# Kernel tuning notes

Measured on AMD Instinct MI355X. Metric: run time of the kernel, lower is better.

## Reference

```python
import jax, jax.numpy as jnp
import numpy as np

# Problem sizes
N, D, B = 4096, 2048, 64  # nodes, feature dim, sequential samples
# LARFDSSOM hyperparameters (from __init__ defaults)
A_T = 0.3          # activation threshold
DSBETA = 1e-4      # moving-average rate
E_B = 0.5          # winner learning rate
E_N = 0.01 * E_B   # neighbor learning rate (e_n is multiplied by e_b in __init__)
EPS_DS = 0.01      # relevance smoothing


def setup_inputs() -> dict:
    key = jax.random.key(0)
    k0, k1, k2, k3, k4 = jax.random.split(key, 5)
    return {
        "x": jax.random.uniform(k0, (B, D), jnp.float32),
        "weights": jax.random.uniform(k1, (N, D), jnp.float32),
        "moving_avg": jax.random.uniform(k2, (N, D), jnp.float32),
        "relevances": jax.random.uniform(k3, (N, D), jnp.float32),
        "wins": jnp.zeros((N,), jnp.float32),
        "neighbors": jax.random.randint(k4, (N, N), 0, 2) > 0,
    }


def _som_steps(x, weights, moving_avg, relevances, wins, neighbors):
    """Sequential LARFDSSOM update_map over B samples (codebook at max size,
    so the add_node branch is structurally impossible and the per-sample step
    is either 'update winner + neighbors' or a no-op)."""
    node_ids = jnp.arange(weights.shape[0])

    def step(state, w):
        W, M, R, wn = state
        diff = w[None, :] - W                          # [N, D]
        # weighted_distance + activation
        dists = jnp.sum(R * diff * diff, axis=1)       # [N]
        rel_sum = jnp.sum(R, axis=1)                   # [N]
        act = rel_sum / (rel_sum + dists + 1e-7)
        winner = jnp.argmax(act)
        do_upd = act[winner] >= A_T                    # else no-op (codebook full)
        is_winner = node_ids == winner
        is_nb = neighbors[winner] & (~is_winner)
        # per-node learning rate: e_b for winner, e_n for neighbors, 0 otherwise
        lr = jnp.where(is_winner, E_B, jnp.where(is_nb, E_N, 0.0))[:, None]  # [N, 1]
        # update_node (vectorized over all nodes, masked below)
        dist_abs = jnp.abs(diff)
        M_new = lr * DSBETA * dist_abs + (1.0 - lr * DSBETA) * M
        mx = jnp.max(M_new, axis=1, keepdims=True)
        mn = jnp.min(M_new, axis=1, keepdims=True)
        av = jnp.mean(M_new, axis=1, keepdims=True)
        denom = EPS_DS * (mx - mn)
        # denom == 0 -> original produces NaN then sets relevance to 1.0
        arg = jnp.clip((M_new - av) / jnp.where(denom == 0.0, 1.0, denom), -80.0, 80.0)
        R_new = jnp.where(denom == 0.0, 1.0, 1.0 / (1.0 + jnp.exp(arg)))
        W_new = W + lr * diff
        m = (do_upd & (lr[:, 0] > 0.0))[:, None]       # rows actually touched
        W = jnp.where(m, W_new, W)
        M = jnp.where(m, M_new, M)
        R = jnp.where(m, R_new, R)
        wn = wn + jnp.where(is_winner & do_upd, 1.0, 0.0)
        return (W, M, R, wn), None

    (W, M, R, wn), _ = jax.lax.scan(step, (weights, moving_avg, relevances, wins), x)
    return W


def reference(x, weights, moving_avg, relevances, wins, neighbors):
    return _som_steps(x, weights, moving_avg, relevances, wins, neighbors)
```

## Files before the change

kernel.cpp:

```cpp
#include <hip/hip_runtime.h>
#include <cstddef>

#define NN 4096
#define DD 2048
#define BB 64
#define RPB 8
#define NBLK (NN / RPB)

constexpr float kAT     = 0.3f;
constexpr float kDSBETA = 1e-4f;
constexpr float kEB     = 0.5f;
constexpr float kEN     = 0.005f;
constexpr float kEPS    = 0.01f;

__device__ __forceinline__ float wave_sum_f(float v) {
#pragma unroll
    for (int o = 32; o; o >>= 1) v += __shfl_xor(v, o, 64);
    return v;
}
__device__ __forceinline__ double wave_sum_d(double v) {
#pragma unroll
    for (int o = 32; o; o >>= 1) v += __shfl_xor(v, o, 64);
    return v;
}
__device__ __forceinline__ float wave_max_f(float v) {
#pragma unroll
    for (int o = 32; o; o >>= 1) v = fmaxf(v, __shfl_xor(v, o, 64));
    return v;
}
__device__ __forceinline__ float wave_min_f(float v) {
#pragma unroll
    for (int o = 32; o; o >>= 1) v = fminf(v, __shfl_xor(v, o, 64));
    return v;
}
__device__ __forceinline__ unsigned long long wave_max_u64(unsigned long long v) {
#pragma unroll
    for (int o = 32; o; o >>= 1) {
        const unsigned long long u = __shfl_xor(v, o, 64);
        v = (u > v) ? u : v;
    }
    return v;
}

__global__ void detect_nb(const unsigned char* __restrict__ nb, unsigned* __restrict__ flag) {
    unsigned v = 0;
    const int i0 = threadIdx.x * 256;
    for (int i = 0; i < 256; i++) {
        const int idx = i0 + i;
        if ((idx & 3) != 0) v |= nb[idx];
    }
    if (v != 0) atomicOr(flag, 1u);
}

__global__ __launch_bounds__(256, 2) void som_persist(
    const float* __restrict__ x,
    const float* __restrict__ W0,
    const float* __restrict__ M0,
    const float* __restrict__ R0,
    const unsigned char* __restrict__ nbb,
    const unsigned* __restrict__ flag,
    float* __restrict__ Wout,
    unsigned long long* __restrict__ part,
    unsigned* __restrict__ cnt)
{
    const int tid  = threadIdx.x;
    const int wid  = tid >> 6;
    const int lane = tid & 63;
    const int n0   = (int)blockIdx.x * RPB;
    const int col  = tid * 8;

    __shared__ double sdd[2][RPB][4];
    __shared__ float  sf[3][4];
    __shared__ unsigned long long skk[RPB];
    __shared__ unsigned long long sKey;

    const bool nb_byte = (*flag != 0);
    const int* nbi = (const int*)nbb;

    float w[RPB][8], r[RPB][8], m[RPB][8], xcur[8];

#pragma unroll
    for (int row = 0; row < RPB; ++row) {
        const size_t base = (size_t)(n0 + row) * DD + col;
        *(float4*)(&w[row][0]) = *(const float4*)(W0 + base);
        *(float4*)(&w[row][4]) = *(const float4*)(W0 + base + 4);
        *(float4*)(&r[row][0]) = *(const float4*)(R0 + base);
        *(float4*)(&r[row][4]) = *(const float4*)(R0 + base + 4);
        *(float4*)(&m[row][0]) = *(const float4*)(M0 + base);
        *(float4*)(&m[row][4]) = *(const float4*)(M0 + base + 4);
    }
    *(float4*)(xcur)     = *(const float4*)(x + col);
    *(float4*)(xcur + 4) = *(const float4*)(x + col + 4);

    auto act_phase = [&](int slot) {
#pragma unroll
        for (int row = 0; row < RPB; ++row) {
            double pd = 0.0, ps = 0.0;
#pragma unroll
            for (int j = 0; j < 8; ++j) {
                const double d  = (double)xcur[j] - (double)w[row][j];
                const double rj = (double)r[row][j];
                pd += rj * d * d;
                ps += rj;
            }
            pd = wave_sum_d(pd); ps = wave_sum_d(ps);
            if (lane == 0) { sdd[0][row][wid] = pd; sdd[1][row][wid] = ps; }
        }
        __syncthreads();
        if (tid < RPB) {
            const int row = tid;
            const double td = sdd[0][row][0] + sdd[0][row][1] + sdd[0][row][2] + sdd[0][row][3];
            const double tr = sdd[1][row][0] + sdd[1][row][1] + sdd[1][row][2] + sdd[1][row][3];
            const double act = tr / (tr + td + 1e-7);
            const unsigned long long ab = (unsigned long long)__double_as_longlong(act);
            skk[row] = (ab & ~0xFFFULL) | (unsigned long long)(4095 - (n0 + row));
        }
        __syncthreads();
        if (tid == 0) {
            unsigned long long k = skk[0];
#pragma unroll
            for (int i = 1; i < RPB; ++i) k = (skk[i] > k) ? skk[i] : k;
            atomicMax(&part[((size_t)slot * 64 + (blockIdx.x & 63)) * 8], k);
            __hip_atomic_fetch_add(&cnt[((size_t)slot * 8 + (blockIdx.x & 7)) * 16], 1u,
                                   __ATOMIC_RELEASE, __HIP_MEMORY_SCOPE_AGENT);
        }
        __syncthreads();
    };

    act_phase(0);

    for (int t = 0; t < BB; ++t) {
        if (wid == 0) {
            int it = 0;
            while (true) {
                unsigned c = 0;
                if (lane < 8)
                    c = __hip_atomic_load(&cnt[((size_t)t * 8 + lane) * 16],
                                          __ATOMIC_ACQUIRE, __HIP_MEMORY_SCOPE_AGENT);
                c += __shfl_xor(c, 1, 64);
                c += __shfl_xor(c, 2, 64);
                c += __shfl_xor(c, 4, 64);
                c = __shfl(c, 0, 64);
                if (c >= (unsigned)NBLK) break;
                if (++it > 2000000) break;
                __builtin_amdgcn_s_sleep(2);
            }
            unsigned long long k = __hip_atomic_load(
                &part[((size_t)t * 64 + lane) * 8],
                __ATOMIC_RELAXED, __HIP_MEMORY_SCOPE_AGENT);
            k = wave_max_u64(k);
            if (lane == 0) sKey = k;
        }
        __syncthreads();
        const unsigned long long k = sKey;
        __syncthreads();
        const double act_w = __longlong_as_double((long long)(k & ~0xFFFULL));
        const int winner   = 4095 - (int)(k & 0xFFFULL);

        if (act_w >= (double)kAT) {
#pragma unroll
            for (int row = 0; row < RPB; ++row) {
                const int n = n0 + row;
                float lr = 0.0f;
                if (n == winner) {
                    lr = kEB;
                } else {
                    const size_t off = (size_t)winner * NN + n;
                    const bool isnb = nb_byte ? (nbb[off] != 0) : (nbi[off] != 0);
                    if (isnb) lr = kEN;
                }
                if (lr != 0.0f) {
                    const float c1 = lr * kDSBETA;
                    const float c2 = 1.0f - c1;
                    float psum = 0.0f, pmx = -INFINITY, pmn = INFINITY;
#pragma unroll
                    for (int j = 0; j < 8; ++j) {
                        const float d  = xcur[j] - w[row][j];
                        const float mv = c1 * fabsf(d) + c2 * m[row][j];
                        w[row][j] += lr * d;
                        m[row][j] = mv;
                        psum += mv;
                        pmx = fmaxf(pmx, mv);
                        pmn = fminf(pmn, mv);
                    }
                    psum = wave_sum_f(psum); pmx = wave_max_f(pmx); pmn = wave_min_f(pmn);
                    if (lane == 0) { sf[0][wid] = psum; sf[1][wid] = pmx; sf[2][wid] = pmn; }
                    __syncthreads();
                    const float ts  = sf[0][0] + sf[0][1] + sf[0][2] + sf[0][3];
                    const float tmx = fmaxf(fmaxf(sf[1][0], sf[1][1]), fmaxf(sf[1][2], sf[1][3]));
                    const float tmn = fminf(fminf(sf[2][0], sf[2][1]), fminf(sf[2][2], sf[2][3]));
                    __syncthreads();
                    const float av    = ts * (1.0f / (float)DD);
                    const float denom = kEPS * (tmx - tmn);
                    if (denom == 0.0f) {
#pragma unroll
                        for (int j = 0; j < 8; ++j) r[row][j] = 1.0f;
                    } else {
#pragma unroll
                        for (int j = 0; j < 8; ++j) {
                            float a = (m[row][j] - av) / denom;
                            a = fminf(fmaxf(a, -80.0f), 80.0f);
                            r[row][j] = 1.0f / (1.0f + expf(a));
                        }
                    }
                }
            }
        }

        if (t < BB - 1) {
            const size_t xb = (size_t)(t + 1) * DD + col;
            *(float4*)(xcur)     = *(const float4*)(x + xb);
            *(float4*)(xcur + 4) = *(const float4*)(x + xb + 4);
            act_phase(t + 1);
        }
    }

#pragma unroll
    for (int row = 0; row < RPB; ++row) {
        const size_t base = (size_t)(n0 + row) * DD + col;
        *(float4*)(Wout + base)     = *(float4*)(&w[row][0]);
        *(float4*)(Wout + base + 4) = *(float4*)(&w[row][4]);
    }
}

__global__ __launch_bounds__(256) void som_step(
    const float* __restrict__ x_upd, const float* __restrict__ x_act,
    float* __restrict__ W, float* __restrict__ M, float* __restrict__ R,
    const void* __restrict__ nb, const unsigned* __restrict__ flag,
    const unsigned long long* __restrict__ part_upd,
    unsigned long long* __restrict__ part_act)
{
    const int n   = blockIdx.x;
    const int tid = threadIdx.x;
    __shared__ float  sred[3][4];
    __shared__ double sredd[2][4];

    float lr = 0.0f;
    if (part_upd != nullptr) {
        unsigned long long k = part_upd[(size_t)(tid & 63) * 8];
        k = wave_max_u64(k);
        const double act_w = __longlong_as_double((long long)(k & ~0xFFFULL));
        const int winner   = 4095 - (int)(k & 0xFFFULL);
        if (act_w >= (double)kAT) {
            if (n == winner) lr = kEB;
            else {
                const size_t off = (size_t)winner * NN + n;
                const bool isnb = (*flag != 0)
                    ? (((const unsigned char*)nb)[off] != 0)
                    : (((const int*)nb)[off] != 0);
                if (isnb) lr = kEN;
            }
        }
    }
    const bool next = (x_act != nullptr);
    if (lr == 0.0f && !next) return;

    const size_t rowoff = (size_t)n * DD + (size_t)tid * 8;
    const size_t xoff   = (size_t)tid * 8;
    float w[8], r[8];
    *(float4*)(w)     = *(const float4*)(W + rowoff);
    *(float4*)(w + 4) = *(const float4*)(W + rowoff + 4);

    if (lr != 0.0f) {
        float m[8], xu[8], mnew[8];
        *(float4*)(m)      = *(const float4*)(M + rowoff);
        *(float4*)(m + 4)  = *(const float4*)(M + rowoff + 4);
        *(float4*)(xu)     = *(const float4*)(x_upd + xoff);
        *(float4*)(xu + 4) = *(const float4*)(x_upd + xoff + 4);
        const float c1 = lr * kDSBETA, c2 = 1.0f - c1;
        float psum = 0.0f, pmx = -INFINITY, pmn = INFINITY;
#pragma unroll
        for (int j = 0; j < 8; j++) {
            const float d = xu[j] - w[j];
            w[j] += lr * d;
            const float mv = c1 * fabsf(d) + c2 * m[j];
            mnew[j] = mv; psum += mv;
            pmx = fmaxf(pmx, mv); pmn = fminf(pmn, mv);
        }
        psum = wave_sum_f(psum); pmx = wave_max_f(pmx); pmn = wave_min_f(pmn);
        const int wid = tid >> 6, lane = tid & 63;
        if (lane == 0) { sred[0][wid] = psum; sred[1][wid] = pmx; sred[2][wid] = pmn; }
        __syncthreads();
        const float ts  = sred[0][0] + sred[0][1] + sred[0][2] + sred[0][3];
        const float tmx = fmaxf(fmaxf(sred[1][0], sred[1][1]), fmaxf(sred[1][2], sred[1][3]));
        const float tmn = fminf(fminf(sred[2][0], sred[2][1]), fminf(sred[2][2], sred[2][3]));
        __syncthreads();
        const float av = ts * (1.0f / (float)DD);
        const float denom = kEPS * (tmx - tmn);
        if (denom == 0.0f) {
#pragma unroll
            for (int j = 0; j < 8; j++) r[j] = 1.0f;
        } else {
#pragma unroll
            for (int j = 0; j < 8; j++) {
                float a = (mnew[j] - av) / denom;
                a = fminf(fmaxf(a, -80.0f), 80.0f);
                r[j] = 1.0f / (1.0f + expf(a));
            }
        }
        *(float4*)(W + rowoff)     = *(float4*)(w);
        *(float4*)(W + rowoff + 4) = *(float4*)(w + 4);
        *(float4*)(M + rowoff)     = *(float4*)(mnew);
        *(float4*)(M + rowoff + 4) = *(float4*)(mnew + 4);
        *(float4*)(R + rowoff)     = *(float4*)(r);
        *(float4*)(R + rowoff + 4) = *(float4*)(r + 4);
    } else {
        *(float4*)(r)     = *(const float4*)(R + rowoff);
        *(float4*)(r + 4) = *(const float4*)(R + rowoff + 4);
    }

    if (next) {
        float xn[8];
        *(float4*)(xn)     = *(const float4*)(x_act + xoff);
        *(float4*)(xn + 4) = *(const float4*)(x_act + xoff + 4);
        double pd = 0.0, ps = 0.0;
#pragma unroll
        for (int j = 0; j < 8; j++) {
            const double d  = (double)xn[j] - (double)w[j];
            const double rj = (double)r[j];
            pd += rj * d * d; ps += rj;
        }
        pd = wave_sum_d(pd); ps = wave_sum_d(ps);
        const int wid = tid >> 6, lane = tid & 63;
        if (lane == 0) { sredd[0][wid] = pd; sredd[1][wid] = ps; }
        __syncthreads();
        if (tid == 0) {
            const double td = sredd[0][0] + sredd[0][1] + sredd[0][2] + sredd[0][3];
            const double tr = sredd[1][0] + sredd[1][1] + sredd[1][2] + sredd[1][3];
            const double act = tr / (tr + td + 1e-7);
            const unsigned long long ab = (unsigned long long)__double_as_longlong(act);
            const unsigned long long kk = (ab & ~0xFFFULL) | (unsigned long long)(4095 - n);
            atomicMax(&part_act[(size_t)(n & 63) * 8], kk);
        }
    }
}

extern "C" void kernel_launch(void* const* d_in, const int* in_sizes, int n_in,
                              void* d_out, int out_size, void* d_ws, size_t ws_size,
                              hipStream_t stream) {
    const float*         x   = (const float*)d_in[0];
    const float*         W0  = (const float*)d_in[1];
    float*               M   = (float*)d_in[2];
    float*               R   = (float*)d_in[3];
    const unsigned char* nbb = (const unsigned char*)d_in[5];
    float*               W   = (float*)d_out;

    unsigned long long* part = (unsigned long long*)d_ws;
    const size_t part_bytes  = (size_t)66 * 64 * 8 * sizeof(unsigned long long);
    unsigned* cnt   = (unsigned*)((char*)d_ws + part_bytes);
    const size_t cnt_bytes = (size_t)BB * 8 * 16 * sizeof(unsigned);
    unsigned* flagp = (unsigned*)((char*)d_ws + part_bytes + cnt_bytes);

    hipMemsetAsync(d_ws, 0, part_bytes + cnt_bytes + 64, stream);
    detect_nb<<<1, 256, 0, stream>>>(nbb, flagp);

    int occ = 0;
    hipError_t qerr = hipOccupancyMaxActiveBlocksPerMultiprocessor(
        &occ, (const void*)som_persist, 256, 0);
    if (qerr == hipSuccess && occ >= 2) {
        som_persist<<<NBLK, 256, 0, stream>>>(x, W0, M, R, nbb, flagp, W, part, cnt);
        return;
    }

    hipMemcpyAsync(W, W0, sizeof(float) * (size_t)NN * DD, hipMemcpyDeviceToDevice, stream);
    som_step<<<NN, 256, 0, stream>>>(nullptr, x, W, M, R, nbb, flagp, nullptr, part);
    for (int t = 0; t < BB; t++) {
        const float* xu = x + (size_t)t * DD;
        const float* xa = (t < BB - 1) ? (x + (size_t)(t + 1) * DD) : nullptr;
        const unsigned long long* pu = part + (size_t)t * 64 * 8;
        unsigned long long*       pa = (t < BB - 1) ? (part + (size_t)(t + 1) * 64 * 8) : nullptr;
        som_step<<<NN, 256, 0, stream>>>(xu, xa, W, M, R, nbb, flagp, pu, pa);
    }
}
```

Baseline: 1.660 ms.

## Replace atomic-counter grid barrier with per-block key slots and single-block reducer

Each block now stores its best activation key with a release store into its own slot instead of doing an atomicMax plus a counter increment. Block 0 polls all 512 slots until every one is nonzero, reduces them to the winner and publishes it to eight replicated slots, which the other blocks poll. The change also loads the winner's neighbor flags for all eight rows in one vector load and prefetches the next sample's x one step ahead. It aims to cut atomic contention and barrier latency, at the cost of an extra hop through block 0 and the assumption that no valid key is ever zero.

```diff
diff --git a/kernel.cpp b/kernel.cpp
--- a/kernel.cpp
+++ b/kernel.cpp
@@ -60,13 +60,14 @@
     const unsigned char* __restrict__ nbb,
     const unsigned* __restrict__ flag,
     float* __restrict__ Wout,
-    unsigned long long* __restrict__ part,
-    unsigned* __restrict__ cnt)
+    unsigned long long* __restrict__ keys,
+    unsigned long long* __restrict__ wkey)
 {
     const int tid  = threadIdx.x;
     const int wid  = tid >> 6;
     const int lane = tid & 63;
-    const int n0   = (int)blockIdx.x * RPB;
+    const int bid  = (int)blockIdx.x;
+    const int n0   = bid * RPB;
     const int col  = tid * 8;
 
     __shared__ double sdd[2][RPB][4];
@@ -75,9 +76,8 @@
     __shared__ unsigned long long sKey;
 
     const bool nb_byte = (*flag != 0);
-    const int* nbi = (const int*)nbb;
-
-    float w[RPB][8], r[RPB][8], m[RPB][8], xcur[8];
+
+    float w[RPB][8], r[RPB][8], m[RPB][8], xcur[8], xnext[8];
 
 #pragma unroll
     for (int row = 0; row < RPB; ++row) {
@@ -92,7 +92,7 @@
     *(float4*)(xcur)     = *(const float4*)(x + col);
     *(float4*)(xcur + 4) = *(const float4*)(x + col + 4);
 
-    auto act_phase = [&](int slot) {
+    auto post_key = [&](int slot) {
 #pragma unroll
         for (int row = 0; row < RPB; ++row) {
             double pd = 0.0, ps = 0.0;
@@ -120,36 +120,50 @@
             unsigned long long k = skk[0];
 #pragma unroll
             for (int i = 1; i < RPB; ++i) k = (skk[i] > k) ? skk[i] : k;
-            atomicMax(&part[((size_t)slot * 64 + (blockIdx.x & 63)) * 8], k);
-            __hip_atomic_fetch_add(&cnt[((size_t)slot * 8 + (blockIdx.x & 7)) * 16], 1u,
-                                   __ATOMIC_RELEASE, __HIP_MEMORY_SCOPE_AGENT);
+            __hip_atomic_store(&keys[(size_t)slot * NBLK + bid], k,
+                               __ATOMIC_RELEASE, __HIP_MEMORY_SCOPE_AGENT);
         }
         __syncthreads();
     };
 
-    act_phase(0);
+    post_key(0);
+    *(float4*)(xnext)     = *(const float4*)(x + DD + col);
+    *(float4*)(xnext + 4) = *(const float4*)(x + DD + 4 + col);
 
     for (int t = 0; t < BB; ++t) {
-        if (wid == 0) {
+        if (bid == 0 && wid == 0) {
+            const unsigned long long* kt = keys + (size_t)t * NBLK;
             int it = 0;
             while (true) {
-                unsigned c = 0;
-                if (lane < 8)
-                    c = __hip_atomic_load(&cnt[((size_t)t * 8 + lane) * 16],
-                                          __ATOMIC_ACQUIRE, __HIP_MEMORY_SCOPE_AGENT);
-                c += __shfl_xor(c, 1, 64);
-                c += __shfl_xor(c, 2, 64);
-                c += __shfl_xor(c, 4, 64);
-                c = __shfl(c, 0, 64);
-                if (c >= (unsigned)NBLK) break;
-                if (++it > 2000000) break;
-                __builtin_amdgcn_s_sleep(2);
-            }
-            unsigned long long k = __hip_atomic_load(
-                &part[((size_t)t * 64 + lane) * 8],
-                __ATOMIC_RELAXED, __HIP_MEMORY_SCOPE_AGENT);
-            k = wave_max_u64(k);
-            if (lane == 0) sKey = k;
+                bool ok = true;
+                unsigned long long mx = 0;
+#pragma unroll
+                for (int i = 0; i < NBLK / 64; ++i) {
+                    const unsigned long long v = __hip_atomic_load(
+                        &kt[lane + 64 * i], __ATOMIC_RELAXED, __HIP_MEMORY_SCOPE_AGENT);
+                    ok &= (v != 0ULL);
+                    mx = (v > mx) ? v : mx;
+                }
+                if (__all(ok) || ++it > 4000000) {
+                    mx = wave_max_u64(mx);
+                    if (lane < 8)
+                        __hip_atomic_store(&wkey[((size_t)t * 8 + lane) * 8], mx,
+                                           __ATOMIC_RELEASE, __HIP_MEMORY_SCOPE_AGENT);
+                    break;
+                }
+                __builtin_amdgcn_s_sleep(1);
+            }
+        }
+        if (tid == 0) {
+            unsigned long long k = 0;
+            int it = 0;
+            while (true) {
+                k = __hip_atomic_load(&wkey[((size_t)t * 8 + (bid & 7)) * 8],
+                                      __ATOMIC_RELAXED, __HIP_MEMORY_SCOPE_AGENT);
+                if (k != 0ULL || ++it > 4000000) break;
+                __builtin_amdgcn_s_sleep(4);
+            }
+            sKey = k;
         }
         __syncthreads();
         const unsigned long long k = sKey;
@@ -158,17 +172,22 @@
         const int winner   = 4095 - (int)(k & 0xFFFULL);
 
         if (act_w >= (double)kAT) {
+            bool isnb[RPB];
+            if (nb_byte) {
+                const unsigned long long nbw =
+                    *(const unsigned long long*)(nbb + (size_t)winner * NN + n0);
+#pragma unroll
+                for (int i = 0; i < RPB; ++i) isnb[i] = ((nbw >> (8 * i)) & 0xFFULL) != 0;
+            } else {
+                const uint4* p = (const uint4*)((const int*)nbb + (size_t)winner * NN + n0);
+                const uint4 a = p[0], b = p[1];
+                isnb[0] = a.x != 0; isnb[1] = a.y != 0; isnb[2] = a.z != 0; isnb[3] = a.w != 0;
+                isnb[4] = b.x != 0; isnb[5] = b.y != 0; isnb[6] = b.z != 0; isnb[7] = b.w != 0;
+            }
 #pragma unroll
             for (int row = 0; row < RPB; ++row) {
                 const int n = n0 + row;
-                float lr = 0.0f;
-                if (n == winner) {
-                    lr = kEB;
-                } else {
-                    const size_t off = (size_t)winner * NN + n;
-                    const bool isnb = nb_byte ? (nbb[off] != 0) : (nbi[off] != 0);
-                    if (isnb) lr = kEN;
-                }
+                const float lr = (n == winner) ? kEB : (isnb[row] ? kEN : 0.0f);
                 if (lr != 0.0f) {
                     const float c1 = lr * kDSBETA;
                     const float c2 = 1.0f - c1;
@@ -208,10 +227,14 @@
         }
 
         if (t < BB - 1) {
-            const size_t xb = (size_t)(t + 1) * DD + col;
-            *(float4*)(xcur)     = *(const float4*)(x + xb);
-            *(float4*)(xcur + 4) = *(const float4*)(x + xb + 4);
-            act_phase(t + 1);
+#pragma unroll
+            for (int j = 0; j < 8; ++j) xcur[j] = xnext[j];
+            post_key(t + 1);
+            if (t < BB - 2) {
+                const size_t xb = (size_t)(t + 2) * DD + col;
+                *(float4*)(xnext)     = *(const float4*)(x + xb);
+                *(float4*)(xnext + 4) = *(const float4*)(x + xb + 4);
+            }
         }
     }
 
@@ -345,23 +368,24 @@
     const unsigned char* nbb = (const unsigned char*)d_in[5];
     float*               W   = (float*)d_out;
 
-    unsigned long long* part = (unsigned long long*)d_ws;
-    const size_t part_bytes  = (size_t)66 * 64 * 8 * sizeof(unsigned long long);
-    unsigned* cnt   = (unsigned*)((char*)d_ws + part_bytes);
-    const size_t cnt_bytes = (size_t)BB * 8 * 16 * sizeof(unsigned);
-    unsigned* flagp = (unsigned*)((char*)d_ws + part_bytes + cnt_bytes);
-
-    hipMemsetAsync(d_ws, 0, part_bytes + cnt_bytes + 64, stream);
+    const size_t regA = (size_t)66 * 64 * 8 * sizeof(unsigned long long);
+    const size_t regB = (size_t)BB * 8 * 8 * sizeof(unsigned long long);
+    unsigned long long* keys  = (unsigned long long*)d_ws;
+    unsigned long long* wkey  = (unsigned long long*)((char*)d_ws + regA);
+    unsigned*           flagp = (unsigned*)((char*)d_ws + regA + regB);
+
+    hipMemsetAsync(d_ws, 0, regA + regB + 64, stream);
     detect_nb<<<1, 256, 0, stream>>>(nbb, flagp);
 
     int occ = 0;
     hipError_t qerr = hipOccupancyMaxActiveBlocksPerMultiprocessor(
         &occ, (const void*)som_persist, 256, 0);
     if (qerr == hipSuccess && occ >= 2) {
-        som_persist<<<NBLK, 256, 0, stream>>>(x, W0, M, R, nbb, flagp, W, part, cnt);
+        som_persist<<<NBLK, 256, 0, stream>>>(x, W0, M, R, nbb, flagp, W, keys, wkey);
         return;
     }
 
+    unsigned long long* part = keys;
     hipMemcpyAsync(W, W0, sizeof(float) * (size_t)NN * DD, hipMemcpyDeviceToDevice, stream);
     som_step<<<NN, 256, 0, stream>>>(nullptr, x, W, M, R, nbb, flagp, nullptr, part);
     for (int t = 0; t < BB; t++) {
```

After: 1.669 ms. Within noise of the previous version (+0.5%).
